# Performance work log

Measured on AMD Instinct MI355X. Metric: run time of the kernel, lower is better.

Reference implementation:

```python
import jax, jax.numpy as jnp
import numpy as np


def setup_inputs() -> dict:
    key = jax.random.key(0)
    k1, k2, k3 = jax.random.split(key, 3)
    B, C, H, W = 8, 128, 128, 128
    kh, kw = 5, 5
    x = jax.random.normal(k1, (B, C, H, W), dtype=jnp.float32)
    weight = jax.random.normal(k2, (B, C, kh, kw), dtype=jnp.float32)
    bias = jax.random.normal(k3, (B, C), dtype=jnp.float32)
    return {"x": x, "weight": weight, "bias": bias, "padding": 2, "stride": 1}


def reference(x, weight, bias, padding, stride):
    # Morphological dilation with external SE: out = max_k(x_patch + w_k) + bias.
    # torch unfold zero-pads, so padded zeros legitimately participate in the max-plus.
    B, C, H, W = x.shape
    kh, kw = weight.shape[-2:]
    ph = pw = int(padding)
    sh = sw = int(stride)
    H2 = (H + 2 * ph - kh) // sh + 1
    W2 = (W + 2 * pw - kw) // sw + 1
    xp = jnp.pad(x, ((0, 0), (0, 0), (ph, ph), (pw, pw)))
    y = None
    # Fixed small kh*kw loop; each iter is a vectorized shifted-window max-plus.
    for di in range(kh):
        for dj in range(kw):
            patch = xp[:, :, di:di + sh * H2:sh, dj:dj + sw * W2:sw]  # B,C,H2,W2
            val = patch + weight[:, :, di, dj][:, :, None, None]
            y = val if y is None else jnp.maximum(y, val)
    return y + bias[:, :, None, None]
```

## Files before the change

kernel.cpp:

```cpp
#include <hip/hip_runtime.h>


static constexpr int H = 128, W = 128, KH = 5, KW = 5, PAD = 2;
static constexpr int RBAND = 32;
static constexpr int NBANDS = H / RBAND;

#define MAX3(a, b, c) fmaxf(fmaxf((a), (b)), (c))

__global__ __launch_bounds__(128) void dilation_kernel(
    const float* __restrict__ x,
    const float* __restrict__ wgt,
    const float* __restrict__ bias,
    float* __restrict__ out)
{
    const int plane = blockIdx.x / NBANDS;
    const int band  = blockIdx.x % NBANDS;
    const int j = threadIdx.x;

    const float* __restrict__ xp = x   + (size_t)plane * (H * W);
    float*       __restrict__ op = out + (size_t)plane * (H * W);
    const float* __restrict__ wp = wgt + plane * (KH * KW);

    float wk[KH][KW];
#pragma unroll
    for (int r = 0; r < KH; ++r)
#pragma unroll
        for (int c = 0; c < KW; ++c)
            wk[r][c] = wp[r * KW + c];
    const float bi = bias[plane];

    int  colc[KW];
    bool colok[KW];
#pragma unroll
    for (int c = 0; c < KW; ++c) {
        int col = j + c - PAD;
        colok[c] = (col >= 0) && (col < W);
        colc[c]  = min(max(col, 0), W - 1);
    }

    const int i0 = band * RBAND;

    float win[KH][KW];

#pragma unroll
    for (int t = 0; t < KH - 1; ++t) {
        const int row   = i0 - PAD + t;
        const bool rowok = (row >= 0) && (row < H);
        const int rowc  = min(max(row, 0), H - 1);
        const float* rp = xp + rowc * W;
#pragma unroll
        for (int c = 0; c < KW; ++c)
            win[t][c] = (rowok && colok[c]) ? rp[colc[c]] : 0.0f;
    }

#pragma unroll
    for (int ii = 0; ii < RBAND; ++ii) {
        const int i = i0 + ii;

        {
            const int row   = i + PAD;
            const bool rowok = (row < H);
            const int rowc  = min(row, H - 1);
            const float* rp = xp + rowc * W;
            const int slot  = (ii + KH - 1) % KH;
#pragma unroll
            for (int c = 0; c < KW; ++c)
                win[slot][c] = (rowok && colok[c]) ? rp[colc[c]] : 0.0f;
        }

        float v[KH * KW];
#pragma unroll
        for (int r = 0; r < KH; ++r) {
            const int s = (ii + r) % KH;
#pragma unroll
            for (int c = 0; c < KW; ++c)
                v[r * KW + c] = win[s][c] + wk[r][c];
        }

        const float u0 = MAX3(v[0],  v[1],  v[2]);
        const float u1 = MAX3(v[3],  v[4],  v[5]);
        const float u2 = MAX3(v[6],  v[7],  v[8]);
        const float u3 = MAX3(v[9],  v[10], v[11]);
        const float u4 = MAX3(v[12], v[13], v[14]);
        const float u5 = MAX3(v[15], v[16], v[17]);
        const float u6 = MAX3(v[18], v[19], v[20]);
        const float u7 = MAX3(v[21], v[22], v[23]);
        const float w0 = MAX3(u0, u1, u2);
        const float w1 = MAX3(u3, u4, u5);
        const float w2 = MAX3(u6, u7, v[24]);
        const float m  = MAX3(w0, w1, w2);

        op[i * W + j] = m + bi;
    }
}

extern "C" void kernel_launch(void* const* d_in, const int* in_sizes, int n_in,
                              void* d_out, int out_size, void* d_ws, size_t ws_size,
                              hipStream_t stream) {
    const float* x    = (const float*)d_in[0];
    const float* wgt  = (const float*)d_in[1];
    const float* bias = (const float*)d_in[2];
    float* out        = (float*)d_out;

    const int planes = in_sizes[2];
    dim3 grid(planes * NBANDS);
    dim3 block(W);
    dilation_kernel<<<grid, block, 0, stream>>>(x, wgt, bias, out);
}
```

Before: 135.9 us.

## Compute four output columns per thread with vectorized row loads and stores

Each thread now produces a 4-wide column group over an 8-row strip, loading each input row as float2+float4+float2 instead of five scalar loads, and writing outputs as float4. Bias is folded into the weights once per thread. Blocks grow to 256 threads covering 64-row bands. This cuts load instruction count and redundant halo reads per output, at the cost of more register pressure and a shorter sliding-window reuse per strip (4 halo rows per 8 outputs).

```diff
diff --git a/kernel.cpp b/kernel.cpp
--- a/kernel.cpp
+++ b/kernel.cpp
@@ -2,96 +2,106 @@
 
 
 static constexpr int H = 128, W = 128, KH = 5, KW = 5, PAD = 2;
-static constexpr int RBAND = 32;
-static constexpr int NBANDS = H / RBAND;
+static constexpr int RSTRIP = 8;
+static constexpr int RBAND  = 64;
+static constexpr int BANDS  = H / RBAND;
 
 #define MAX3(a, b, c) fmaxf(fmaxf((a), (b)), (c))
 
-__global__ __launch_bounds__(128) void dilation_kernel(
+__global__ __launch_bounds__(256) void dilation_kernel(
     const float* __restrict__ x,
     const float* __restrict__ wgt,
     const float* __restrict__ bias,
     float* __restrict__ out)
 {
-    const int plane = blockIdx.x / NBANDS;
-    const int band  = blockIdx.x % NBANDS;
-    const int j = threadIdx.x;
+    const int plane = blockIdx.x / BANDS;
+    const int band  = blockIdx.x % BANDS;
+    const int tid = threadIdx.x;
+    const int cg  = tid & 31;
+    const int rs  = tid >> 5;
+    const int j0  = cg * 4;
+    const int base = band * RBAND + rs * RSTRIP;
 
     const float* __restrict__ xp = x   + (size_t)plane * (H * W);
     float*       __restrict__ op = out + (size_t)plane * (H * W);
     const float* __restrict__ wp = wgt + plane * (KH * KW);
 
-    float wk[KH][KW];
+    const float bi = bias[plane];
+    float wk[KH * KW];
 #pragma unroll
-    for (int r = 0; r < KH; ++r)
-#pragma unroll
-        for (int c = 0; c < KW; ++c)
-            wk[r][c] = wp[r * KW + c];
-    const float bi = bias[plane];
+    for (int i = 0; i < KH * KW; ++i) wk[i] = wp[i] + bi;
 
-    int  colc[KW];
-    bool colok[KW];
-#pragma unroll
-    for (int c = 0; c < KW; ++c) {
-        int col = j + c - PAD;
-        colok[c] = (col >= 0) && (col < W);
-        colc[c]  = min(max(col, 0), W - 1);
-    }
+    const bool cgL = (cg > 0);
+    const bool cgR = (cg < 31);
+    const int colL = cgL ? (j0 - 2) : 0;
+    const int colR = cgR ? (j0 + 4) : (W - 2);
 
-    const int i0 = band * RBAND;
+    float win[KH][8];
 
-    float win[KH][KW];
+#define LOAD_ROW(SLOT, ROW, ROK)                                              \
+    do {                                                                      \
+        const bool rok_ = (ROK);                                              \
+        const int  rowc_ = rok_ ? (ROW) : 0;                                  \
+        const float* rp_ = xp + rowc_ * W;                                    \
+        const float2 L_ = *reinterpret_cast<const float2*>(rp_ + colL);       \
+        const float4 M_ = *reinterpret_cast<const float4*>(rp_ + j0);         \
+        const float2 R_ = *reinterpret_cast<const float2*>(rp_ + colR);       \
+        win[SLOT][0] = (rok_ && cgL) ? L_.x : 0.0f;                           \
+        win[SLOT][1] = (rok_ && cgL) ? L_.y : 0.0f;                           \
+        win[SLOT][2] = rok_ ? M_.x : 0.0f;                                    \
+        win[SLOT][3] = rok_ ? M_.y : 0.0f;                                    \
+        win[SLOT][4] = rok_ ? M_.z : 0.0f;                                    \
+        win[SLOT][5] = rok_ ? M_.w : 0.0f;                                    \
+        win[SLOT][6] = (rok_ && cgR) ? R_.x : 0.0f;                           \
+        win[SLOT][7] = (rok_ && cgR) ? R_.y : 0.0f;                           \
+    } while (0)
 
 #pragma unroll
     for (int t = 0; t < KH - 1; ++t) {
-        const int row   = i0 - PAD + t;
-        const bool rowok = (row >= 0) && (row < H);
-        const int rowc  = min(max(row, 0), H - 1);
-        const float* rp = xp + rowc * W;
-#pragma unroll
-        for (int c = 0; c < KW; ++c)
-            win[t][c] = (rowok && colok[c]) ? rp[colc[c]] : 0.0f;
+        const int row = base - PAD + t;
+        LOAD_ROW(t, row, row >= 0);
     }
 
 #pragma unroll
-    for (int ii = 0; ii < RBAND; ++ii) {
-        const int i = i0 + ii;
+    for (int it = 0; it < RSTRIP; ++it) {
+        const int i = base + it;
 
         {
-            const int row   = i + PAD;
-            const bool rowok = (row < H);
-            const int rowc  = min(row, H - 1);
-            const float* rp = xp + rowc * W;
-            const int slot  = (ii + KH - 1) % KH;
-#pragma unroll
-            for (int c = 0; c < KW; ++c)
-                win[slot][c] = (rowok && colok[c]) ? rp[colc[c]] : 0.0f;
+            const int row = i + PAD;
+            const int slot = (it + KH - 1) % KH;
+            LOAD_ROW(slot, row < H ? row : (H - 1), row < H);
         }
 
-        float v[KH * KW];
+        float res[4];
 #pragma unroll
-        for (int r = 0; r < KH; ++r) {
-            const int s = (ii + r) % KH;
+        for (int k = 0; k < 4; ++k) {
+            float v[KH * KW];
 #pragma unroll
-            for (int c = 0; c < KW; ++c)
-                v[r * KW + c] = win[s][c] + wk[r][c];
+            for (int r = 0; r < KH; ++r) {
+                const int s = (it + r) % KH;
+#pragma unroll
+                for (int c = 0; c < KW; ++c)
+                    v[r * KW + c] = win[s][k + c] + wk[r * KW + c];
+            }
+            const float u0 = MAX3(v[0],  v[1],  v[2]);
+            const float u1 = MAX3(v[3],  v[4],  v[5]);
+            const float u2 = MAX3(v[6],  v[7],  v[8]);
+            const float u3 = MAX3(v[9],  v[10], v[11]);
+            const float u4 = MAX3(v[12], v[13], v[14]);
+            const float u5 = MAX3(v[15], v[16], v[17]);
+            const float u6 = MAX3(v[18], v[19], v[20]);
+            const float u7 = MAX3(v[21], v[22], v[23]);
+            const float w0 = MAX3(u0, u1, u2);
+            const float w1 = MAX3(u3, u4, u5);
+            const float w2 = MAX3(u6, u7, v[24]);
+            res[k] = MAX3(w0, w1, w2);
         }
 
-        const float u0 = MAX3(v[0],  v[1],  v[2]);
-        const float u1 = MAX3(v[3],  v[4],  v[5]);
-        const float u2 = MAX3(v[6],  v[7],  v[8]);
-        const float u3 = MAX3(v[9],  v[10], v[11]);
-        const float u4 = MAX3(v[12], v[13], v[14]);
-        const float u5 = MAX3(v[15], v[16], v[17]);
-        const float u6 = MAX3(v[18], v[19], v[20]);
-        const float u7 = MAX3(v[21], v[22], v[23]);
-        const float w0 = MAX3(u0, u1, u2);
-        const float w1 = MAX3(u3, u4, u5);
-        const float w2 = MAX3(u6, u7, v[24]);
-        const float m  = MAX3(w0, w1, w2);
-
-        op[i * W + j] = m + bi;
+        float4 o;
+        o.x = res[0]; o.y = res[1]; o.z = res[2]; o.w = res[3];
+        *reinterpret_cast<float4*>(op + i * W + j0) = o;
     }
+#undef LOAD_ROW
 }
 
 extern "C" void kernel_launch(void* const* d_in, const int* in_sizes, int n_in,
@@ -103,7 +113,7 @@
     float* out        = (float*)d_out;
 
     const int planes = in_sizes[2];
-    dim3 grid(planes * NBANDS);
-    dim3 block(W);
+    dim3 grid(planes * BANDS);
+    dim3 block(256);
     dilation_kernel<<<grid, block, 0, stream>>>(x, wgt, bias, out);
 }
```

New measurement: 126.7 us. 1.07x faster.
